# Performance work log

Hardware: AMD Instinct MI355X
Metric: run time of the kernel (lower is better)

## Reference

```python
import jax, jax.numpy as jnp
import numpy as np

NUM_HEADS = 8
EPS = 1e-6


def setup_inputs() -> dict:
    key = jax.random.key(0)
    k1, k2, k3 = jax.random.split(key, 3)
    B, N, C = 4, 256, 512
    x = jax.random.normal(k1, (B, N, C), dtype=jnp.float32)
    w_qkv = jax.random.normal(k2, (3 * C, C), dtype=jnp.float32) * (C ** -0.5)
    w_proj = jax.random.normal(k3, (C, C), dtype=jnp.float32) * (C ** -0.5)
    b_proj = jnp.zeros((C,), dtype=jnp.float32)
    paramR = jnp.ones((1,), dtype=jnp.float32)
    return {"x": x, "w_qkv": w_qkv, "w_proj": w_proj, "b_proj": b_proj, "paramR": paramR}


def _fourier_attention(x, w_qkv, w_proj, b_proj, paramR):
    B, N, C = x.shape
    H = NUM_HEADS
    Dh = C // H
    # qkv projection (no bias), split into per-head q,k,v: (B,H,N,Dh)
    qkv = jnp.einsum('bnc,kc->bnk', x, w_qkv).reshape(B, N, 3, H, Dh)
    q = qkv[:, :, 0].transpose(0, 2, 1, 3)
    k = qkv[:, :, 1].transpose(0, 2, 1, 3)
    v = qkv[:, :, 2].transpose(0, 2, 1, 3)
    R = paramR[0]
    # Generalized Fourier integral kernel: prod_d sin(R*(q_d - k_d))/(q_d - k_d)
    diff = q[:, :, :, None, :] - k[:, :, None, :, :]  # (B,H,Nq,Nk,Dh)
    near0 = jnp.abs(diff) < 1e-8
    safe = jnp.where(near0, jnp.float32(1.0), diff)
    s = jnp.where(near0, R, jnp.sin(R * safe) / safe)
    score = jnp.prod(s, axis=-1)  # (B,H,Nq,Nk)
    a4 = score ** 4
    attn = a4 / (jnp.sum(a4, axis=-1, keepdims=True) + EPS)  # normalize over keys
    out = jnp.einsum('bhqk,bhkd->bhqd', attn, v)
    out = out.transpose(0, 2, 1, 3).reshape(B, N, C)
    return jnp.einsum('bnc,oc->bno', out, w_proj) + b_proj


def reference(x, w_qkv, w_proj, b_proj, paramR):
    return _fourier_attention(x, w_qkv, w_proj, b_proj, paramR)
```

## Files before the change

### kernel.cpp

```cpp
#include <hip/hip_runtime.h>
#include <math.h>

#define BB 4
#define NN 256
#define CC 512
#define HH 8
#define DH 64

typedef __attribute__((ext_vector_type(8))) short bf16x8;
typedef __attribute__((ext_vector_type(4))) float f32x4;

__device__ inline unsigned short f2bf(float f) {
  unsigned u = __float_as_uint(f);
  u += 0x7FFFu + ((u >> 16) & 1u);
  return (unsigned short)(u >> 16);
}
__device__ inline float bf2f(unsigned short s) {
  return __uint_as_float((unsigned)s << 16);
}

__global__ __launch_bounds__(256) void cvt_hilo(
    const float* __restrict__ in, unsigned short* __restrict__ h,
    unsigned short* __restrict__ l, int n) {
  int i = (blockIdx.x * 256 + threadIdx.x) * 4;
  if (i >= n) return;
  float4 f = *(const float4*)(in + i);
  float fa[4] = {f.x, f.y, f.z, f.w};
  ushort4 hv, lv;
  unsigned short* hp = (unsigned short*)&hv;
  unsigned short* lp = (unsigned short*)&lv;
#pragma unroll
  for (int j = 0; j < 4; j++) {
    unsigned short hb = f2bf(fa[j]);
    hp[j] = hb;
    lp[j] = f2bf(fa[j] - bf2f(hb));
  }
  *(ushort4*)(h + i) = hv;
  *(ushort4*)(l + i) = lv;
}

template <bool BIAS>
__global__ __launch_bounds__(256, 2) void gemm_mfma(
    const unsigned short* __restrict__ Ah, const unsigned short* __restrict__ Al,
    const unsigned short* __restrict__ Bh, const unsigned short* __restrict__ Bl,
    const float* __restrict__ bias, float* __restrict__ C, int M, int N,
    int K) {
  __shared__ unsigned short sAh[128][40], sAl[128][40];
  __shared__ unsigned short sBh[128][40], sBl[128][40];
  const int t = threadIdx.x;
  const int lane = t & 63;
  const int w = t >> 6;
  const int bm = blockIdx.y * 128;
  const int bn = blockIdx.x * 128;
  const int wr = (w >> 1) * 64;
  const int wc = (w & 1) * 64;
  const int quad = lane >> 4;
  const int l16 = lane & 15;

  f32x4 acc[4][4];
#pragma unroll
  for (int i = 0; i < 4; i++)
#pragma unroll
    for (int j = 0; j < 4; j++) {
      acc[i][j][0] = 0.f;
      acc[i][j][1] = 0.f;
      acc[i][j][2] = 0.f;
      acc[i][j][3] = 0.f;
    }

  for (int k0 = 0; k0 < K; k0 += 32) {
    __syncthreads();
#pragma unroll
    for (int s = 0; s < 2; s++) {
      int slot = t + 256 * s;
      int r = slot >> 2;
      int c8 = (slot & 3) * 8;
      *(uint4*)&sAh[r][c8] = *(const uint4*)(Ah + (size_t)(bm + r) * K + k0 + c8);
      *(uint4*)&sAl[r][c8] = *(const uint4*)(Al + (size_t)(bm + r) * K + k0 + c8);
      *(uint4*)&sBh[r][c8] = *(const uint4*)(Bh + (size_t)(bn + r) * K + k0 + c8);
      *(uint4*)&sBl[r][c8] = *(const uint4*)(Bl + (size_t)(bn + r) * K + k0 + c8);
    }
    __syncthreads();

    bf16x8 ah[4], al[4], bh[4], bl[4];
#pragma unroll
    for (int i = 0; i < 4; i++) {
      ah[i] = *(const bf16x8*)&sAh[wr + i * 16 + l16][quad * 8];
      al[i] = *(const bf16x8*)&sAl[wr + i * 16 + l16][quad * 8];
      bh[i] = *(const bf16x8*)&sBh[wc + i * 16 + l16][quad * 8];
      bl[i] = *(const bf16x8*)&sBl[wc + i * 16 + l16][quad * 8];
    }
#pragma unroll
    for (int i = 0; i < 4; i++)
#pragma unroll
      for (int j = 0; j < 4; j++) {
        acc[i][j] = __builtin_amdgcn_mfma_f32_16x16x32_bf16(ah[i], bh[j],
                                                            acc[i][j], 0, 0, 0);
        acc[i][j] = __builtin_amdgcn_mfma_f32_16x16x32_bf16(ah[i], bl[j],
                                                            acc[i][j], 0, 0, 0);
        acc[i][j] = __builtin_amdgcn_mfma_f32_16x16x32_bf16(al[i], bh[j],
                                                            acc[i][j], 0, 0, 0);
      }
  }

#pragma unroll
  for (int i = 0; i < 4; i++)
#pragma unroll
    for (int j = 0; j < 4; j++) {
      int n = bn + wc + j * 16 + l16;
      float bv = BIAS ? bias[n] : 0.f;
#pragma unroll
      for (int r = 0; r < 4; r++) {
        int m = bm + wr + i * 16 + quad * 4 + r;
        C[(size_t)m * N + n] = acc[i][j][r] + bv;
      }
    }
}

__global__ __launch_bounds__(512, 4) void fourier_attn(
    const float* __restrict__ qkv, const float* __restrict__ paramR,
    unsigned short* __restrict__ aoh, unsigned short* __restrict__ aol) {
  __shared__ float Kt[64][68];
  __shared__ float VtT[64][68];
  __shared__ float Qs[16][DH];
  __shared__ float A4[8][64][2];

  const int t = threadIdx.x;
  const int lane = t & 63;
  const int wv = t >> 6;
  const int qc = blockIdx.x;
  const int h = blockIdx.y;
  const int b = blockIdx.z;
  const float R = paramR[0];

  const float* base = qkv + (size_t)b * NN * (3 * CC) + h * DH;

  if (t < 256) {
    int r = t >> 4;
    int c4 = (t & 15) << 2;
    *(float4*)&Qs[r][c4] =
        *(const float4*)(base + (size_t)(qc * 16 + r) * (3 * CC) + c4);
  }

  const int qi0 = wv * 2, qi1 = wv * 2 + 1;
  float Sp[2] = {0.f, 0.f};
  float acc[2] = {0.f, 0.f};

  for (int jt = 0; jt < 4; jt++) {
    __syncthreads();
#pragma unroll
    for (int u0 = 0; u0 < 2; u0++) {
      int u = t + 512 * u0;
      int r = u >> 4;
      int c4 = (u & 15) << 2;
      const float* krow = base + (size_t)(jt * 64 + r) * (3 * CC) + CC;
      *(float4*)&Kt[r][c4] = *(const float4*)(krow + c4);
      const float* vrow = base + (size_t)(jt * 64 + r) * (3 * CC) + 2 * CC;
      float4 vv = *(const float4*)(vrow + c4);
      VtT[c4 + 0][r] = vv.x;
      VtT[c4 + 1][r] = vv.y;
      VtT[c4 + 2][r] = vv.z;
      VtT[c4 + 3][r] = vv.w;
    }
    __syncthreads();

    float nm[2][2] = {{1.f, 1.f}, {1.f, 1.f}};
    float dn[2][2] = {{1.f, 1.f}, {1.f, 1.f}};
#pragma unroll
    for (int d4 = 0; d4 < 16; d4++) {
      const int p = d4 & 1;
      float4 k4 = *(const float4*)&Kt[lane][4 * d4];
      float4 qa = *(const float4*)&Qs[qi0][4 * d4];
      float4 qb = *(const float4*)&Qs[qi1][4 * d4];
      float ka[4] = {k4.x, k4.y, k4.z, k4.w};
      float q0a[4] = {qa.x, qa.y, qa.z, qa.w};
      float q1a[4] = {qb.x, qb.y, qb.z, qb.w};
#pragma unroll
      for (int j = 0; j < 4; j++) {
        float d0 = q0a[j] - ka[j] + 1e-30f;
        float d1 = q1a[j] - ka[j] + 1e-30f;
        nm[0][p] *= __sinf(R * d0);
        dn[0][p] *= d0;
        nm[1][p] *= __sinf(R * d1);
        dn[1][p] *= d1;
      }
    }
#pragma unroll
    for (int q = 0; q < 2; q++) {
      float sc = (nm[q][0] * nm[q][1]) / (dn[q][0] * dn[q][1]);
      float s2 = sc * sc;
      float a4 = s2 * s2;
      Sp[q] += a4;
      A4[wv][lane][q] = a4;
    }

#pragma unroll
    for (int j4 = 0; j4 < 16; j4++) {
      float4 v4 = *(const float4*)&VtT[lane][4 * j4];
      float4 a01 = *(const float4*)&A4[wv][4 * j4 + 0][0];
      float4 a23 = *(const float4*)&A4[wv][4 * j4 + 2][0];
      acc[0] = fmaf(a01.x, v4.x, acc[0]);
      acc[1] = fmaf(a01.y, v4.x, acc[1]);
      acc[0] = fmaf(a01.z, v4.y, acc[0]);
      acc[1] = fmaf(a01.w, v4.y, acc[1]);
      acc[0] = fmaf(a23.x, v4.z, acc[0]);
      acc[1] = fmaf(a23.y, v4.z, acc[1]);
      acc[0] = fmaf(a23.z, v4.w, acc[0]);
      acc[1] = fmaf(a23.w, v4.w, acc[1]);
    }
  }

#pragma unroll
  for (int q = 0; q < 2; q++) {
    float s = Sp[q];
#pragma unroll
    for (int off = 32; off > 0; off >>= 1) s += __shfl_xor(s, off, 64);
    float o = acc[q] / (s + 1e-6f);
    int n = qc * 16 + wv * 2 + q;
    size_t idx = (size_t)(b * NN + n) * CC + h * DH + lane;
    unsigned short oh = f2bf(o);
    aoh[idx] = oh;
    aol[idx] = f2bf(o - bf2f(oh));
  }
}

extern "C" void kernel_launch(void* const* d_in, const int* in_sizes, int n_in,
                              void* d_out, int out_size, void* d_ws,
                              size_t ws_size, hipStream_t stream) {
  const float* x = (const float*)d_in[0];
  const float* w_qkv = (const float*)d_in[1];
  const float* w_proj = (const float*)d_in[2];
  const float* b_proj = (const float*)d_in[3];
  const float* paramR = (const float*)d_in[4];
  float* outp = (float*)d_out;

  const int nX = BB * NN * CC;
  const int nWq = 3 * CC * CC;
  const int nWp = CC * CC;

  unsigned short* xh = (unsigned short*)d_ws;
  unsigned short* xl = xh + nX;
  unsigned short* wqh = xl + nX;
  unsigned short* wql = wqh + nWq;
  unsigned short* wph = wql + nWq;
  unsigned short* wpl = wph + nWp;
  unsigned short* aoh = wpl + nWp;
  unsigned short* aol = aoh + nX;
  float* qkv_ws = (float*)(aol + nX);

  cvt_hilo<<<nX / 1024, 256, 0, stream>>>(x, xh, xl, nX);
  cvt_hilo<<<nWq / 1024, 256, 0, stream>>>(w_qkv, wqh, wql, nWq);
  cvt_hilo<<<nWp / 1024, 256, 0, stream>>>(w_proj, wph, wpl, nWp);

  gemm_mfma<false><<<dim3(3 * CC / 128, BB * NN / 128), 256, 0, stream>>>(
      xh, xl, wqh, wql, nullptr, qkv_ws, BB * NN, 3 * CC, CC);

  fourier_attn<<<dim3(NN / 16, HH, BB), 512, 0, stream>>>(qkv_ws, paramR, aoh,
                                                          aol);

  gemm_mfma<true><<<dim3(CC / 128, BB * NN / 128), 256, 0, stream>>>(
      aoh, aol, wph, wpl, b_proj, outp, BB * NN, CC, CC);
}
```

Baseline: 150.3 us.

## Split attention over key halves, shrink GEMM tiles, fuse conversion kernels

The three hi/lo bf16 conversion launches become one combined kernel. Both GEMMs move to small 32-row tiles, so more blocks run concurrently. The attention kernel splits the keys into two halves per query chunk, doubling the grid, and writes partial outputs and sums that a new normalize kernel combines before the hi/lo split. It also pre-scales q and k by R so R leaves the inner loop, and XOR-swizzles K and V in shared memory to cut bank conflicts. The cost is an extra launch, extra global traffic for the partials, and a different zero-difference edge case (the result is 0 when the denominator is zero, where the reference uses R).

Result: slower. 571.9 us (+280.5%).

```diff
diff --git a/kernel.cpp b/kernel.cpp
--- a/kernel.cpp
+++ b/kernel.cpp
@@ -19,12 +19,25 @@
   return __uint_as_float((unsigned)s << 16);
 }
 
-__global__ __launch_bounds__(256) void cvt_hilo(
-    const float* __restrict__ in, unsigned short* __restrict__ h,
-    unsigned short* __restrict__ l, int n) {
+__global__ __launch_bounds__(256) void cvt_all(
+    const float* __restrict__ x, const float* __restrict__ wq,
+    const float* __restrict__ wp, unsigned short* __restrict__ xh,
+    unsigned short* __restrict__ xl, unsigned short* __restrict__ wqh,
+    unsigned short* __restrict__ wql, unsigned short* __restrict__ wph,
+    unsigned short* __restrict__ wpl) {
+  const int nX = BB * NN * CC, nWq = 3 * CC * CC;
   int i = (blockIdx.x * 256 + threadIdx.x) * 4;
-  if (i >= n) return;
-  float4 f = *(const float4*)(in + i);
+  const float* src;
+  unsigned short *dh, *dl;
+  int off;
+  if (i < nX) {
+    src = x; dh = xh; dl = xl; off = i;
+  } else if (i < nX + nWq) {
+    src = wq; dh = wqh; dl = wql; off = i - nX;
+  } else {
+    src = wp; dh = wph; dl = wpl; off = i - nX - nWq;
+  }
+  float4 f = *(const float4*)(src + off);
   float fa[4] = {f.x, f.y, f.z, f.w};
   ushort4 hv, lv;
   unsigned short* hp = (unsigned short*)&hv;
@@ -35,132 +48,140 @@
     hp[j] = hb;
     lp[j] = f2bf(fa[j] - bf2f(hb));
   }
-  *(ushort4*)(h + i) = hv;
-  *(ushort4*)(l + i) = lv;
-}
-
-template <bool BIAS>
-__global__ __launch_bounds__(256, 2) void gemm_mfma(
+  *(ushort4*)(dh + off) = hv;
+  *(ushort4*)(dl + off) = lv;
+}
+
+template <int TJ, bool BIAS>
+__global__ __launch_bounds__(256, 4) void gemm_mfma(
     const unsigned short* __restrict__ Ah, const unsigned short* __restrict__ Al,
     const unsigned short* __restrict__ Bh, const unsigned short* __restrict__ Bl,
     const float* __restrict__ bias, float* __restrict__ C, int M, int N,
     int K) {
-  __shared__ unsigned short sAh[128][40], sAl[128][40];
-  __shared__ unsigned short sBh[128][40], sBl[128][40];
+  __shared__ unsigned short sAh[32][40], sAl[32][40];
+  __shared__ unsigned short sBh[32 * TJ][40], sBl[32 * TJ][40];
   const int t = threadIdx.x;
   const int lane = t & 63;
   const int w = t >> 6;
-  const int bm = blockIdx.y * 128;
-  const int bn = blockIdx.x * 128;
-  const int wr = (w >> 1) * 64;
-  const int wc = (w & 1) * 64;
+  const int bm = blockIdx.y * 32;
+  const int bn = blockIdx.x * (32 * TJ);
+  const int wr = (w >> 1) * 16;
+  const int wc = (w & 1) * (16 * TJ);
   const int quad = lane >> 4;
   const int l16 = lane & 15;
 
-  f32x4 acc[4][4];
-#pragma unroll
-  for (int i = 0; i < 4; i++)
-#pragma unroll
-    for (int j = 0; j < 4; j++) {
-      acc[i][j][0] = 0.f;
-      acc[i][j][1] = 0.f;
-      acc[i][j][2] = 0.f;
-      acc[i][j][3] = 0.f;
-    }
+  f32x4 acc[TJ];
+#pragma unroll
+  for (int j = 0; j < TJ; j++) {
+    acc[j][0] = 0.f; acc[j][1] = 0.f; acc[j][2] = 0.f; acc[j][3] = 0.f;
+  }
+
+  const int aHalf = t >> 7;
+  const int aR = (t >> 2) & 31;
+  const int aC8 = (t & 3) * 8;
 
   for (int k0 = 0; k0 < K; k0 += 32) {
     __syncthreads();
-#pragma unroll
-    for (int s = 0; s < 2; s++) {
-      int slot = t + 256 * s;
-      int r = slot >> 2;
-      int c8 = (slot & 3) * 8;
-      *(uint4*)&sAh[r][c8] = *(const uint4*)(Ah + (size_t)(bm + r) * K + k0 + c8);
-      *(uint4*)&sAl[r][c8] = *(const uint4*)(Al + (size_t)(bm + r) * K + k0 + c8);
-      *(uint4*)&sBh[r][c8] = *(const uint4*)(Bh + (size_t)(bn + r) * K + k0 + c8);
-      *(uint4*)&sBl[r][c8] = *(const uint4*)(Bl + (size_t)(bn + r) * K + k0 + c8);
+    {
+      const unsigned short* src =
+          (aHalf ? Al : Ah) + (size_t)(bm + aR) * K + k0 + aC8;
+      uint4 vv = *(const uint4*)src;
+      if (aHalf) *(uint4*)&sAl[aR][aC8] = vv;
+      else       *(uint4*)&sAh[aR][aC8] = vv;
+    }
+#pragma unroll
+    for (int i = 0; i < TJ; i++) {
+      int s = t + 256 * i;
+      int half = s / (128 * TJ);
+      int rem = s % (128 * TJ);
+      int r = rem >> 2;
+      int c8 = (rem & 3) * 8;
+      const unsigned short* src =
+          (half ? Bl : Bh) + (size_t)(bn + r) * K + k0 + c8;
+      uint4 vv = *(const uint4*)src;
+      if (half) *(uint4*)&sBl[r][c8] = vv;
+      else      *(uint4*)&sBh[r][c8] = vv;
     }
     __syncthreads();
 
-    bf16x8 ah[4], al[4], bh[4], bl[4];
-#pragma unroll
-    for (int i = 0; i < 4; i++) {
-      ah[i] = *(const bf16x8*)&sAh[wr + i * 16 + l16][quad * 8];
-      al[i] = *(const bf16x8*)&sAl[wr + i * 16 + l16][quad * 8];
-      bh[i] = *(const bf16x8*)&sBh[wc + i * 16 + l16][quad * 8];
-      bl[i] = *(const bf16x8*)&sBl[wc + i * 16 + l16][quad * 8];
-    }
-#pragma unroll
-    for (int i = 0; i < 4; i++)
-#pragma unroll
-      for (int j = 0; j < 4; j++) {
-        acc[i][j] = __builtin_amdgcn_mfma_f32_16x16x32_bf16(ah[i], bh[j],
-                                                            acc[i][j], 0, 0, 0);
-        acc[i][j] = __builtin_amdgcn_mfma_f32_16x16x32_bf16(ah[i], bl[j],
-                                                            acc[i][j], 0, 0, 0);
-        acc[i][j] = __builtin_amdgcn_mfma_f32_16x16x32_bf16(al[i], bh[j],
-                                                            acc[i][j], 0, 0, 0);
-      }
-  }
-
-#pragma unroll
-  for (int i = 0; i < 4; i++)
-#pragma unroll
-    for (int j = 0; j < 4; j++) {
-      int n = bn + wc + j * 16 + l16;
-      float bv = BIAS ? bias[n] : 0.f;
-#pragma unroll
-      for (int r = 0; r < 4; r++) {
-        int m = bm + wr + i * 16 + quad * 4 + r;
-        C[(size_t)m * N + n] = acc[i][j][r] + bv;
-      }
-    }
-}
-
-__global__ __launch_bounds__(512, 4) void fourier_attn(
+    bf16x8 ah = *(const bf16x8*)&sAh[wr + l16][quad * 8];
+    bf16x8 al = *(const bf16x8*)&sAl[wr + l16][quad * 8];
+#pragma unroll
+    for (int j = 0; j < TJ; j++) {
+      bf16x8 bh = *(const bf16x8*)&sBh[wc + j * 16 + l16][quad * 8];
+      bf16x8 bl = *(const bf16x8*)&sBl[wc + j * 16 + l16][quad * 8];
+      acc[j] = __builtin_amdgcn_mfma_f32_16x16x32_bf16(ah, bh, acc[j], 0, 0, 0);
+      acc[j] = __builtin_amdgcn_mfma_f32_16x16x32_bf16(ah, bl, acc[j], 0, 0, 0);
+      acc[j] = __builtin_amdgcn_mfma_f32_16x16x32_bf16(al, bh, acc[j], 0, 0, 0);
+    }
+  }
+
+#pragma unroll
+  for (int j = 0; j < TJ; j++) {
+    int n = bn + wc + j * 16 + l16;
+    float bv = BIAS ? bias[n] : 0.f;
+#pragma unroll
+    for (int r = 0; r < 4; r++) {
+      int m = bm + wr + quad * 4 + r;
+      C[(size_t)m * N + n] = acc[j][r] + bv;
+    }
+  }
+}
+
+__global__ __launch_bounds__(512, 8) void fourier_attn(
     const float* __restrict__ qkv, const float* __restrict__ paramR,
-    unsigned short* __restrict__ aoh, unsigned short* __restrict__ aol) {
-  __shared__ float Kt[64][68];
-  __shared__ float VtT[64][68];
-  __shared__ float Qs[16][DH];
+    float* __restrict__ acc0, float* __restrict__ acc1,
+    float* __restrict__ S0, float* __restrict__ S1) {
+  __shared__ float Kt[64][64];
+  __shared__ float VtT[64][64];
+  __shared__ float Qs[16][64];
   __shared__ float A4[8][64][2];
 
   const int t = threadIdx.x;
   const int lane = t & 63;
   const int wv = t >> 6;
-  const int qc = blockIdx.x;
+  const int qc = blockIdx.x >> 1;
+  const int ks = blockIdx.x & 1;
   const int h = blockIdx.y;
   const int b = blockIdx.z;
   const float R = paramR[0];
+  const float R64 = __powf(R * R, 32.0f);
 
   const float* base = qkv + (size_t)b * NN * (3 * CC) + h * DH;
 
   if (t < 256) {
     int r = t >> 4;
     int c4 = (t & 15) << 2;
-    *(float4*)&Qs[r][c4] =
-        *(const float4*)(base + (size_t)(qc * 16 + r) * (3 * CC) + c4);
+    float4 qv = *(const float4*)(base + (size_t)(qc * 16 + r) * (3 * CC) + c4);
+    qv.x *= R; qv.y *= R; qv.z *= R; qv.w *= R;
+    *(float4*)&Qs[r][c4] = qv;
   }
 
   const int qi0 = wv * 2, qi1 = wv * 2 + 1;
+  const int sw = lane & 15;
   float Sp[2] = {0.f, 0.f};
-  float acc[2] = {0.f, 0.f};
-
-  for (int jt = 0; jt < 4; jt++) {
+  float oacc[2] = {0.f, 0.f};
+
+  for (int jt2 = 0; jt2 < 2; jt2++) {
+    const int jt = ks * 2 + jt2;
     __syncthreads();
 #pragma unroll
     for (int u0 = 0; u0 < 2; u0++) {
       int u = t + 512 * u0;
       int r = u >> 4;
-      int c4 = (u & 15) << 2;
+      int g = u & 15;
+      int c4 = g << 2;
       const float* krow = base + (size_t)(jt * 64 + r) * (3 * CC) + CC;
-      *(float4*)&Kt[r][c4] = *(const float4*)(krow + c4);
+      float4 kv = *(const float4*)(krow + c4);
+      kv.x *= R; kv.y *= R; kv.z *= R; kv.w *= R;
+      *(float4*)&Kt[r][(g ^ (r & 15)) << 2] = kv;
       const float* vrow = base + (size_t)(jt * 64 + r) * (3 * CC) + 2 * CC;
       float4 vv = *(const float4*)(vrow + c4);
-      VtT[c4 + 0][r] = vv.x;
-      VtT[c4 + 1][r] = vv.y;
-      VtT[c4 + 2][r] = vv.z;
-      VtT[c4 + 3][r] = vv.w;
+      int kg = r >> 2, ko = r & 3;
+      float va[4] = {vv.x, vv.y, vv.z, vv.w};
+#pragma unroll
+      for (int i = 0; i < 4; i++)
+        VtT[c4 + i][((kg ^ ((c4 + i) & 15)) << 2) + ko] = va[i];
     }
     __syncthreads();
 
@@ -169,25 +190,27 @@
 #pragma unroll
     for (int d4 = 0; d4 < 16; d4++) {
       const int p = d4 & 1;
-      float4 k4 = *(const float4*)&Kt[lane][4 * d4];
-      float4 qa = *(const float4*)&Qs[qi0][4 * d4];
-      float4 qb = *(const float4*)&Qs[qi1][4 * d4];
+      float4 k4 = *(const float4*)&Kt[lane][(d4 ^ sw) << 2];
+      float4 qa = *(const float4*)&Qs[qi0][d4 << 2];
+      float4 qb = *(const float4*)&Qs[qi1][d4 << 2];
       float ka[4] = {k4.x, k4.y, k4.z, k4.w};
       float q0a[4] = {qa.x, qa.y, qa.z, qa.w};
       float q1a[4] = {qb.x, qb.y, qb.z, qb.w};
 #pragma unroll
       for (int j = 0; j < 4; j++) {
-        float d0 = q0a[j] - ka[j] + 1e-30f;
-        float d1 = q1a[j] - ka[j] + 1e-30f;
-        nm[0][p] *= __sinf(R * d0);
-        dn[0][p] *= d0;
-        nm[1][p] *= __sinf(R * d1);
-        dn[1][p] *= d1;
+        float D0 = q0a[j] - ka[j];
+        float D1 = q1a[j] - ka[j];
+        nm[0][p] *= __sinf(D0);
+        dn[0][p] *= D0;
+        nm[1][p] *= __sinf(D1);
+        dn[1][p] *= D1;
       }
     }
 #pragma unroll
     for (int q = 0; q < 2; q++) {
-      float sc = (nm[q][0] * nm[q][1]) / (dn[q][0] * dn[q][1]);
+      float num = nm[q][0] * nm[q][1];
+      float den = dn[q][0] * dn[q][1];
+      float sc = (den != 0.f) ? (num / den) * R64 : 0.f;
       float s2 = sc * sc;
       float a4 = s2 * s2;
       Sp[q] += a4;
@@ -195,33 +218,59 @@
     }
 
 #pragma unroll
-    for (int j4 = 0; j4 < 16; j4++) {
-      float4 v4 = *(const float4*)&VtT[lane][4 * j4];
-      float4 a01 = *(const float4*)&A4[wv][4 * j4 + 0][0];
-      float4 a23 = *(const float4*)&A4[wv][4 * j4 + 2][0];
-      acc[0] = fmaf(a01.x, v4.x, acc[0]);
-      acc[1] = fmaf(a01.y, v4.x, acc[1]);
-      acc[0] = fmaf(a01.z, v4.y, acc[0]);
-      acc[1] = fmaf(a01.w, v4.y, acc[1]);
-      acc[0] = fmaf(a23.x, v4.z, acc[0]);
-      acc[1] = fmaf(a23.y, v4.z, acc[1]);
-      acc[0] = fmaf(a23.z, v4.w, acc[0]);
-      acc[1] = fmaf(a23.w, v4.w, acc[1]);
-    }
-  }
-
+    for (int kg = 0; kg < 16; kg++) {
+      float4 v4 = *(const float4*)&VtT[lane][(kg ^ sw) << 2];
+      float4 a01 = *(const float4*)&A4[wv][kg * 4 + 0][0];
+      float4 a23 = *(const float4*)&A4[wv][kg * 4 + 2][0];
+      oacc[0] = fmaf(a01.x, v4.x, oacc[0]);
+      oacc[1] = fmaf(a01.y, v4.x, oacc[1]);
+      oacc[0] = fmaf(a01.z, v4.y, oacc[0]);
+      oacc[1] = fmaf(a01.w, v4.y, oacc[1]);
+      oacc[0] = fmaf(a23.x, v4.z, oacc[0]);
+      oacc[1] = fmaf(a23.y, v4.z, oacc[1]);
+      oacc[0] = fmaf(a23.z, v4.w, oacc[0]);
+      oacc[1] = fmaf(a23.w, v4.w, oacc[1]);
+    }
+  }
+
+  float* accp = ks ? acc1 : acc0;
+  float* Sg = ks ? S1 : S0;
 #pragma unroll
   for (int q = 0; q < 2; q++) {
     float s = Sp[q];
 #pragma unroll
     for (int off = 32; off > 0; off >>= 1) s += __shfl_xor(s, off, 64);
-    float o = acc[q] / (s + 1e-6f);
     int n = qc * 16 + wv * 2 + q;
-    size_t idx = (size_t)(b * NN + n) * CC + h * DH + lane;
-    unsigned short oh = f2bf(o);
-    aoh[idx] = oh;
-    aol[idx] = f2bf(o - bf2f(oh));
-  }
+    accp[(size_t)(b * NN + n) * CC + h * DH + lane] = oacc[q];
+    if (lane == 0) Sg[((b * HH + h) << 8) + n] = s;
+  }
+}
+
+__global__ __launch_bounds__(256) void normalize_hilo(
+    const float* __restrict__ acc0, const float* __restrict__ acc1,
+    const float* __restrict__ S0, const float* __restrict__ S1,
+    unsigned short* __restrict__ aoh, unsigned short* __restrict__ aol) {
+  int idx = (blockIdx.x * 256 + threadIdx.x) * 4;
+  int m = idx >> 9;
+  int c = idx & 511;
+  int b = m >> 8, n = m & 255, h = c >> 6;
+  int si = ((b * HH + h) << 8) + n;
+  float s = S0[si] + S1[si] + 1e-6f;
+  float4 a = *(const float4*)(acc0 + idx);
+  float4 a1 = *(const float4*)(acc1 + idx);
+  float oa[4] = {(a.x + a1.x) / s, (a.y + a1.y) / s, (a.z + a1.z) / s,
+                 (a.w + a1.w) / s};
+  ushort4 hv, lv;
+  unsigned short* hp = (unsigned short*)&hv;
+  unsigned short* lp = (unsigned short*)&lv;
+#pragma unroll
+  for (int j = 0; j < 4; j++) {
+    unsigned short hb = f2bf(oa[j]);
+    hp[j] = hb;
+    lp[j] = f2bf(oa[j] - bf2f(hb));
+  }
+  *(ushort4*)(aoh + idx) = hv;
+  *(ushort4*)(aol + idx) = lv;
 }
 
 extern "C" void kernel_launch(void* const* d_in, const int* in_sizes, int n_in,
@@ -248,16 +297,22 @@
   unsigned short* aol = aoh + nX;
   float* qkv_ws = (float*)(aol + nX);
 
-  cvt_hilo<<<nX / 1024, 256, 0, stream>>>(x, xh, xl, nX);
-  cvt_hilo<<<nWq / 1024, 256, 0, stream>>>(w_qkv, wqh, wql, nWq);
-  cvt_hilo<<<nWp / 1024, 256, 0, stream>>>(w_proj, wph, wpl, nWp);
-
-  gemm_mfma<false><<<dim3(3 * CC / 128, BB * NN / 128), 256, 0, stream>>>(
+  float* acc0 = (float*)d_ws;
+  float* acc1 = acc0 + nX;
+  float* S0 = acc1 + nX;
+  float* S1 = S0 + BB * HH * NN;
+
+  cvt_all<<<(nX + nWq + nWp) / 1024, 256, 0, stream>>>(
+      x, w_qkv, w_proj, xh, xl, wqh, wql, wph, wpl);
+
+  gemm_mfma<2, false><<<dim3(3 * CC / 64, BB * NN / 32), 256, 0, stream>>>(
       xh, xl, wqh, wql, nullptr, qkv_ws, BB * NN, 3 * CC, CC);
 
-  fourier_attn<<<dim3(NN / 16, HH, BB), 512, 0, stream>>>(qkv_ws, paramR, aoh,
-                                                          aol);
-
-  gemm_mfma<true><<<dim3(CC / 128, BB * NN / 128), 256, 0, stream>>>(
+  fourier_attn<<<dim3(32, HH, BB), 512, 0, stream>>>(qkv_ws, paramR, acc0,
+                                                     acc1, S0, S1);
+
+  normalize_hilo<<<nX / 1024, 256, 0, stream>>>(acc0, acc1, S0, S1, aoh, aol);
+
+  gemm_mfma<1, true><<<dim3(CC / 32, BB * NN / 32), 256, 0, stream>>>(
       aoh, aol, wph, wpl, b_proj, outp, BB * NN, CC, CC);
 }
```
